# Optimization experiments

Hardware: AMD Instinct MI355X
Metric: run time of the kernel (lower is better)

## Reference

```python
import jax, jax.numpy as jnp
import numpy as np

EPS = 1e-5
B, NA, T, D, H, L, DFF, E = 4, 64, 128, 128, 8, 3, 512, 65536
NN = T * NA  # nodes per graph = t*n after reshape(b, t*n, f)
DH = D // H


def _layer_norm(x, g, b):
    m = x.mean(-1, keepdims=True)
    v = ((x - m) ** 2).mean(-1, keepdims=True)
    return (x - m) * jax.lax.rsqrt(v + EPS) * g + b


def _pos_encoding(t, d):
    pos = jnp.arange(t, dtype=jnp.float32)[:, None]
    i = jnp.arange(0, d, 2, dtype=jnp.float32)
    ang = pos * jnp.exp(-jnp.log(10000.0) * i / d)
    pe = jnp.zeros((t, d), jnp.float32)
    return pe.at[:, 0::2].set(jnp.sin(ang)).at[:, 1::2].set(jnp.cos(ang))


def _forward(all_hist_feat, edge_weight, hist_w, hist_b,
             attn_wq, attn_bq, attn_wk, attn_bk, attn_wv, attn_bv, attn_wo, attn_bo,
             ln1_g, ln1_b, ff_w1, ff_b1, ff_w2, ff_b2, ln2_g, ln2_b,
             bn_g, bn_b, lin_graph_w, lin_graph_b, edge_index):
    b, n, t, _ = all_hist_feat.shape
    # history embedding: Linear(3, D)  -> [b, n, t, D]
    x = all_hist_feat @ hist_w + hist_b
    # sinusoidal positional encoding over the time axis
    out_e = x + _pos_encoding(t, D)
    scale = 1.0 / jnp.sqrt(jnp.asarray(DH, jnp.float32))
    for l in range(L):  # small fixed layer count
        q = out_e @ attn_wq[l] + attn_bq[l]
        k = out_e @ attn_wk[l] + attn_bk[l]
        v = out_e @ attn_wv[l] + attn_bv[l]
        qh = q.reshape(b, n, t, H, DH)
        kh = k.reshape(b, n, t, H, DH)
        vh = v.reshape(b, n, t, H, DH)
        scores = jnp.einsum('bnqhd,bnkhd->bnhqk', qh, kh) * scale
        attn = jax.nn.softmax(scores, axis=-1)
        o = jnp.einsum('bnhqk,bnkhd->bnqhd', attn, vh).reshape(b, n, t, D)
        o = o @ attn_wo[l] + attn_bo[l]
        h1 = _layer_norm(out_e + o, ln1_g[l], ln1_b[l])
        ff = jax.nn.relu(h1 @ ff_w1[l] + ff_b1[l]) @ ff_w2[l] + ff_b2[l]
        out_e = _layer_norm(h1 + ff, ln2_g[l], ln2_b[l])
    # graph stage: nodes are (time, agent) pairs, index = time*n + agent
    graph_w = out_e.transpose(0, 2, 1, 3).reshape(b, t * n, D)
    graph_x = x.transpose(0, 2, 1, 3).reshape(b, t * n, D)
    # GCNConv_Fixed_W (no self loops, no normalize): per-node score then
    # edge-weighted scatter-add from source to target (PyG convention)
    s = (graph_w * graph_x).sum(-1)  # [b, t*n]
    src, dst = edge_index[:, 0], edge_index[:, 1]

    def agg(s_b, src_b, dst_b, ew_b):
        return jax.ops.segment_sum(ew_b * s_b[src_b], dst_b, num_segments=NN)

    graph_out = jax.vmap(agg)(s, src, dst, edge_weight)  # [b, t*n]
    g = graph_out.reshape(b, t, n)
    # BatchNorm2d(1) on [b, 1, n, t]: single channel -> global batch stats
    m = g.mean()
    var = g.var()
    g = (g - m) * jax.lax.rsqrt(var + EPS) * bn_g[0] + bn_b[0]
    g4 = g.transpose(0, 2, 1)[..., None]  # [b, n, t, 1]
    return g4 @ lin_graph_w + lin_graph_b  # [b, n, t, D]


def setup_inputs() -> dict:
    keys = iter(jax.random.split(jax.random.key(0), 64))

    def nrm(shape, scale):
        return jax.random.normal(next(keys), shape, jnp.float32) * scale

    inp = {
        'all_hist_feat': nrm((B, NA, T, 3), 1.0),
        'edge_index': jax.random.randint(next(keys), (B, 2, E), 0, NN, jnp.int32),
        'edge_weight': jax.random.uniform(next(keys), (B, E), jnp.float32),
        'hist_w': nrm((3, D), 0.5), 'hist_b': nrm((D,), 0.02),
        'attn_wq': nrm((L, D, D), D ** -0.5), 'attn_bq': jnp.zeros((L, D)),
        'attn_wk': nrm((L, D, D), D ** -0.5), 'attn_bk': jnp.zeros((L, D)),
        'attn_wv': nrm((L, D, D), D ** -0.5), 'attn_bv': jnp.zeros((L, D)),
        'attn_wo': nrm((L, D, D), D ** -0.5), 'attn_bo': jnp.zeros((L, D)),
        'ln1_g': jnp.ones((L, D)), 'ln1_b': jnp.zeros((L, D)),
        'ff_w1': nrm((L, D, DFF), D ** -0.5), 'ff_b1': jnp.zeros((L, DFF)),
        'ff_w2': nrm((L, DFF, D), DFF ** -0.5), 'ff_b2': jnp.zeros((L, D)),
        'ln2_g': jnp.ones((L, D)), 'ln2_b': jnp.zeros((L, D)),
        'bn_g': jnp.ones((1,)), 'bn_b': jnp.zeros((1,)),
        'lin_graph_w': nrm((1, D), 1.0), 'lin_graph_b': jnp.zeros((D,)),
    }
    return inp


def reference(all_hist_feat, edge_index, edge_weight, hist_w, hist_b,
              attn_wq, attn_bq, attn_wk, attn_bk, attn_wv, attn_bv, attn_wo, attn_bo,
              ln1_g, ln1_b, ff_w1, ff_b1, ff_w2, ff_b2, ln2_g, ln2_b,
              bn_g, bn_b, lin_graph_w, lin_graph_b):
    return _forward(all_hist_feat, edge_weight, hist_w, hist_b,
                    attn_wq, attn_bq, attn_wk, attn_bk, attn_wv, attn_bv, attn_wo, attn_bo,
                    ln1_g, ln1_b, ff_w1, ff_b1, ff_w2, ff_b2, ln2_g, ln2_b,
                    bn_g, bn_b, lin_graph_w, lin_graph_b, edge_index)
```

## Files before the change

kernel.cpp:

```cpp
#include <hip/hip_runtime.h>
#include <hip/hip_bf16.h>
#include <math.h>

#define EPS_ 1e-5f
constexpr int B_ = 4, NA = 64, T_ = 128, D_ = 128, H_ = 8, L_ = 3, DFF = 512, E_ = 65536;
constexpr int DH = D_ / H_;
constexpr int NN = T_ * NA;
constexpr int NTOT = B_ * NA * T_;
constexpr int QLD = 384;
constexpr size_t NE_ = (size_t)NTOT * D_;

typedef __bf16 bf16x8 __attribute__((ext_vector_type(8)));
typedef float f32x4 __attribute__((ext_vector_type(4)));

__global__ __launch_bounds__(256) void embed_kernel(
    const float* __restrict__ hist, const float* __restrict__ w,
    const float* __restrict__ b, float* __restrict__ x, float* __restrict__ e) {
  int idx = blockIdx.x * 256 + threadIdx.x;
  if (idx >= NTOT * D_) return;
  int d = idx & (D_ - 1);
  int r = idx >> 7;
  int t = r & (T_ - 1);
  const float* hp = hist + (size_t)r * 3;
  float acc = b[d];
  acc += hp[0] * w[0 * D_ + d];
  acc += hp[1] * w[1 * D_ + d];
  acc += hp[2] * w[2 * D_ + d];
  x[idx] = acc;
  int p = d >> 1;
  float ang = (float)t * expf(-logf(10000.f) * (2.f * (float)p) / (float)D_);
  float pe = (d & 1) ? cosf(ang) : sinf(ang);
  e[idx] = acc + pe;
}

__global__ __launch_bounds__(256) void convert_weights(
    const float* __restrict__ wq, const float* __restrict__ wk,
    const float* __restrict__ wv, const float* __restrict__ wo,
    const float* __restrict__ w1, const float* __restrict__ w2,
    __bf16* __restrict__ hi, __bf16* __restrict__ lo) {
  const int LW = 196608;
  int idx = blockIdx.x * 256 + threadIdx.x;
  if (idx >= L_ * LW) return;
  int l = idx / LW;
  int rem = idx - l * LW;
  float src;
  int n, k, K, segoff;
  if (rem < 49152) {
    n = rem >> 7; k = rem & 127; K = 128; segoff = 0;
    int which = n >> 7, nl = n & 127;
    const float* W = (which == 0) ? wq : (which == 1) ? wk : wv;
    src = W[(size_t)l * 16384 + k * 128 + nl];
  } else if (rem < 65536) {
    int r2 = rem - 49152;
    n = r2 >> 7; k = r2 & 127; K = 128; segoff = 49152;
    src = wo[(size_t)l * 16384 + k * 128 + n];
  } else if (rem < 131072) {
    int r2 = rem - 65536;
    n = r2 >> 7; k = r2 & 127; K = 128; segoff = 65536;
    src = w1[(size_t)l * 65536 + k * 512 + n];
  } else {
    int r2 = rem - 131072;
    n = r2 >> 9; k = r2 & 511; K = 512; segoff = 131072;
    src = w2[(size_t)l * 65536 + k * 128 + n];
  }
  int nt = n >> 4, kt = k >> 5;
  int lane = ((k >> 3) & 3) * 16 + (n & 15);
  int j = k & 7;
  int dst = l * LW + segoff + ((nt * (K / 32) + kt) * 64 + lane) * 8 + j;
  __bf16 h = (__bf16)src;
  hi[dst] = h;
  lo[dst] = (__bf16)(src - (float)h);
}

__global__ __launch_bounds__(256) void bias_pack(
    const float* __restrict__ bq, const float* __restrict__ bk,
    const float* __restrict__ bv, float* __restrict__ pb) {
  int idx = blockIdx.x * 256 + threadIdx.x;
  if (idx >= L_ * QLD) return;
  int l = idx / QLD, n = idx - l * QLD;
  int which = n >> 7, nl = n & 127;
  const float* src = (which == 0) ? bq : (which == 1) ? bk : bv;
  pb[idx] = src[l * 128 + nl];
}

__device__ __forceinline__ void split8(const float* __restrict__ p,
                                       bf16x8& hi, bf16x8& lo) {
  float4 x0 = *(const float4*)p;
  float4 x1 = *(const float4*)(p + 4);
  float xv[8] = {x0.x, x0.y, x0.z, x0.w, x1.x, x1.y, x1.z, x1.w};
#pragma unroll
  for (int j = 0; j < 8; ++j) {
    __bf16 h = (__bf16)xv[j];
    hi[j] = h;
    lo[j] = (__bf16)(xv[j] - (float)h);
  }
}

template <int EPI, int K>
__global__ __launch_bounds__(256) void gemm_big(
    const float* __restrict__ A, int lda,
    const __bf16* __restrict__ Whi, const __bf16* __restrict__ Wlo,
    const float* __restrict__ bias,
    float* __restrict__ C, int ldc) {
  const int wave = threadIdx.x >> 6;
  const int lane = threadIdx.x & 63;
  const int m16 = lane & 15;
  const int quad = lane >> 4;
  const int wrow = wave >> 1, wcol = wave & 1;
  const int row0 = blockIdx.y * 128 + wrow * 64;
  const int col0 = blockIdx.x * 128 + wcol * 64;
  const int ctb = col0 >> 4;

  f32x4 acc[4][4] = {};
#pragma unroll
  for (int k0 = 0; k0 < K; k0 += 32) {
    bf16x8 ahi[4], alo[4];
#pragma unroll
    for (int mf = 0; mf < 4; ++mf)
      split8(A + (size_t)(row0 + mf * 16 + m16) * lda + k0 + quad * 8, ahi[mf], alo[mf]);
    bf16x8 bhi[4], blo[4];
#pragma unroll
    for (int nf = 0; nf < 4; ++nf) {
      size_t off = ((size_t)(ctb + nf) * (K / 32) + (k0 >> 5)) * 512 + lane * 8;
      bhi[nf] = *(const bf16x8*)(Whi + off);
      blo[nf] = *(const bf16x8*)(Wlo + off);
    }
#pragma unroll
    for (int mf = 0; mf < 4; ++mf)
#pragma unroll
      for (int nf = 0; nf < 4; ++nf) {
        acc[mf][nf] = __builtin_amdgcn_mfma_f32_16x16x32_bf16(ahi[mf], bhi[nf], acc[mf][nf], 0, 0, 0);
        acc[mf][nf] = __builtin_amdgcn_mfma_f32_16x16x32_bf16(ahi[mf], blo[nf], acc[mf][nf], 0, 0, 0);
        acc[mf][nf] = __builtin_amdgcn_mfma_f32_16x16x32_bf16(alo[mf], bhi[nf], acc[mf][nf], 0, 0, 0);
      }
  }
#pragma unroll
  for (int mf = 0; mf < 4; ++mf)
#pragma unroll
    for (int nf = 0; nf < 4; ++nf) {
      int c = col0 + nf * 16 + m16;
      float bj = bias[c];
#pragma unroll
      for (int reg = 0; reg < 4; ++reg) {
        int r = row0 + mf * 16 + quad * 4 + reg;
        float v = acc[mf][nf][reg] + bj;
        if (EPI == 1) v = fmaxf(v, 0.f);
        C[(size_t)r * ldc + c] = v;
      }
    }
}

template <int K>
__global__ __launch_bounds__(256) void gemm_ln(
    const float* __restrict__ A, int lda,
    const __bf16* __restrict__ Whi, const __bf16* __restrict__ Wlo,
    const float* __restrict__ bias, const float* __restrict__ resid,
    const float* __restrict__ lng, const float* __restrict__ lnb,
    float* __restrict__ C) {
  const int wave = threadIdx.x >> 6;
  const int lane = threadIdx.x & 63;
  const int m16 = lane & 15;
  const int quad = lane >> 4;
  const int wrow = wave >> 1, wcol = wave & 1;
  const int row0 = blockIdx.y * 64 + wrow * 32;
  const int col0 = wcol * 64;
  const int ctb = wcol * 4;

  f32x4 acc[2][4] = {};
#pragma unroll
  for (int k0 = 0; k0 < K; k0 += 32) {
    bf16x8 ahi[2], alo[2];
#pragma unroll
    for (int mf = 0; mf < 2; ++mf)
      split8(A + (size_t)(row0 + mf * 16 + m16) * lda + k0 + quad * 8, ahi[mf], alo[mf]);
    bf16x8 bhi[4], blo[4];
#pragma unroll
    for (int nf = 0; nf < 4; ++nf) {
      size_t off = ((size_t)(ctb + nf) * (K / 32) + (k0 >> 5)) * 512 + lane * 8;
      bhi[nf] = *(const bf16x8*)(Whi + off);
      blo[nf] = *(const bf16x8*)(Wlo + off);
    }
#pragma unroll
    for (int mf = 0; mf < 2; ++mf)
#pragma unroll
      for (int nf = 0; nf < 4; ++nf) {
        acc[mf][nf] = __builtin_amdgcn_mfma_f32_16x16x32_bf16(ahi[mf], bhi[nf], acc[mf][nf], 0, 0, 0);
        acc[mf][nf] = __builtin_amdgcn_mfma_f32_16x16x32_bf16(ahi[mf], blo[nf], acc[mf][nf], 0, 0, 0);
        acc[mf][nf] = __builtin_amdgcn_mfma_f32_16x16x32_bf16(alo[mf], bhi[nf], acc[mf][nf], 0, 0, 0);
      }
  }
  __shared__ float rs[64][2], rq[64][2];
#pragma unroll
  for (int mf = 0; mf < 2; ++mf)
#pragma unroll
    for (int reg = 0; reg < 4; ++reg) {
      int lr = wrow * 32 + mf * 16 + quad * 4 + reg;
      int gr = blockIdx.y * 64 + lr;
      float s = 0.f, qq = 0.f;
#pragma unroll
      for (int nf = 0; nf < 4; ++nf) {
        int c = col0 + nf * 16 + m16;
        float v = acc[mf][nf][reg] + bias[c] + resid[(size_t)gr * 128 + c];
        acc[mf][nf][reg] = v;
        s += v;
        qq += v * v;
      }
#pragma unroll
      for (int off = 1; off < 16; off <<= 1) {
        s += __shfl_xor(s, off, 64);
        qq += __shfl_xor(qq, off, 64);
      }
      if (m16 == 0) { rs[lr][wcol] = s; rq[lr][wcol] = qq; }
    }
  __syncthreads();
#pragma unroll
  for (int mf = 0; mf < 2; ++mf)
#pragma unroll
    for (int reg = 0; reg < 4; ++reg) {
      int lr = wrow * 32 + mf * 16 + quad * 4 + reg;
      int gr = blockIdx.y * 64 + lr;
      float mean = (rs[lr][0] + rs[lr][1]) * (1.f / 128.f);
      float var = (rq[lr][0] + rq[lr][1]) * (1.f / 128.f) - mean * mean;
      float rstd = rsqrtf(var + EPS_);
#pragma unroll
      for (int nf = 0; nf < 4; ++nf) {
        int c = col0 + nf * 16 + m16;
        C[(size_t)gr * 128 + c] = (acc[mf][nf][reg] - mean) * rstd * lng[c] + lnb[c];
      }
    }
}

__global__ __launch_bounds__(256) void gemm_pk(
    const float* __restrict__ A, const __bf16* __restrict__ Whi,
    const __bf16* __restrict__ Wlo, float* __restrict__ P) {
  const int kc = blockIdx.x;
  const int wave = threadIdx.x >> 6;
  const int lane = threadIdx.x & 63;
  const int m16 = lane & 15;
  const int quad = lane >> 4;
  const int wrow = wave >> 1, wcol = wave & 1;
  const int row0 = blockIdx.y * 64 + wrow * 32;
  const int col0 = wcol * 64;
  const int ctb = wcol * 4;

  f32x4 acc[2][4] = {};
#pragma unroll
  for (int kt = 0; kt < 4; ++kt) {
    const int k0 = kc * 128 + kt * 32;
    bf16x8 ahi[2], alo[2];
#pragma unroll
    for (int mf = 0; mf < 2; ++mf)
      split8(A + (size_t)(row0 + mf * 16 + m16) * 512 + k0 + quad * 8, ahi[mf], alo[mf]);
    bf16x8 bhi[4], blo[4];
#pragma unroll
    for (int nf = 0; nf < 4; ++nf) {
      size_t off = ((size_t)(ctb + nf) * 16 + (k0 >> 5)) * 512 + lane * 8;
      bhi[nf] = *(const bf16x8*)(Whi + off);
      blo[nf] = *(const bf16x8*)(Wlo + off);
    }
#pragma unroll
    for (int mf = 0; mf < 2; ++mf)
#pragma unroll
      for (int nf = 0; nf < 4; ++nf) {
        acc[mf][nf] = __builtin_amdgcn_mfma_f32_16x16x32_bf16(ahi[mf], bhi[nf], acc[mf][nf], 0, 0, 0);
        acc[mf][nf] = __builtin_amdgcn_mfma_f32_16x16x32_bf16(ahi[mf], blo[nf], acc[mf][nf], 0, 0, 0);
        acc[mf][nf] = __builtin_amdgcn_mfma_f32_16x16x32_bf16(alo[mf], bhi[nf], acc[mf][nf], 0, 0, 0);
      }
  }
  float* out = P + (size_t)kc * NE_;
#pragma unroll
  for (int mf = 0; mf < 2; ++mf)
#pragma unroll
    for (int nf = 0; nf < 4; ++nf) {
      int c = col0 + nf * 16 + m16;
#pragma unroll
      for (int reg = 0; reg < 4; ++reg) {
        int r = row0 + mf * 16 + quad * 4 + reg;
        out[(size_t)r * 128 + c] = acc[mf][nf][reg];
      }
    }
}

__global__ __launch_bounds__(128) void reduce_ln4(
    const float* __restrict__ P, const float* __restrict__ bias,
    const float* __restrict__ resid,
    const float* __restrict__ gam, const float* __restrict__ bet,
    float* __restrict__ out) {
  int r = blockIdx.x;
  int d = threadIdx.x;
  size_t o = (size_t)r * D_ + d;
  float val = P[o] + P[o + NE_] + P[o + 2 * NE_] + P[o + 3 * NE_] + bias[d] + resid[o];
  __shared__ float red[4];
  float s = val;
#pragma unroll
  for (int off = 32; off; off >>= 1) s += __shfl_down(s, off, 64);
  if ((d & 63) == 0) red[d >> 6] = s;
  __syncthreads();
  float mean = (red[0] + red[1]) * (1.f / (float)D_);
  float dv = val - mean;
  float q = dv * dv;
#pragma unroll
  for (int off = 32; off; off >>= 1) q += __shfl_down(q, off, 64);
  if ((d & 63) == 0) red[2 + (d >> 6)] = q;
  __syncthreads();
  float var = (red[2] + red[3]) * (1.f / (float)D_);
  out[o] = dv * rsqrtf(var + EPS_) * gam[d] + bet[d];
}

__global__ __launch_bounds__(256) void attn_mfma(float* __restrict__ qkv) {
  const int h = blockIdx.x & (H_ - 1);
  const int bn = blockIdx.x >> 3;
  const int wave = threadIdx.x >> 6;
  const int lane = threadIdx.x & 63;
  const int m16 = lane & 15;
  const int quad = lane >> 4;
  const int row0 = wave * 32;
  const float* Qb = qkv + (size_t)bn * T_ * QLD + h * DH;
  const float* Kb = Qb + 128;
  const float* Vb = Qb + 256;
  float* Ob = (float*)Vb;

  __shared__ __bf16 Plds[4][32][136];

  bf16x8 qhi[2], qlo[2];
#pragma unroll
  for (int mf = 0; mf < 2; ++mf) {
    if (quad < 2) {
      split8(Qb + (size_t)(row0 + mf * 16 + m16) * QLD + quad * 8, qhi[mf], qlo[mf]);
    } else {
#pragma unroll
      for (int j = 0; j < 8; ++j) { qhi[mf][j] = (__bf16)0.f; qlo[mf][j] = (__bf16)0.f; }
    }
  }

  f32x4 acc[2][8] = {};
#pragma unroll
  for (int nf = 0; nf < 8; ++nf) {
    bf16x8 khi, klo;
    if (quad < 2) {
      split8(Kb + (size_t)(nf * 16 + m16) * QLD + quad * 8, khi, klo);
    } else {
#pragma unroll
      for (int j = 0; j < 8; ++j) { khi[j] = (__bf16)0.f; klo[j] = (__bf16)0.f; }
    }
#pragma unroll
    for (int mf = 0; mf < 2; ++mf) {
      acc[mf][nf] = __builtin_amdgcn_mfma_f32_16x16x32_bf16(qhi[mf], khi, acc[mf][nf], 0, 0, 0);
      acc[mf][nf] = __builtin_amdgcn_mfma_f32_16x16x32_bf16(qhi[mf], klo, acc[mf][nf], 0, 0, 0);
      acc[mf][nf] = __builtin_amdgcn_mfma_f32_16x16x32_bf16(qlo[mf], khi, acc[mf][nf], 0, 0, 0);
    }
  }

  const float scale = 0.25f;
#pragma unroll
  for (int mf = 0; mf < 2; ++mf)
#pragma unroll
    for (int reg = 0; reg < 4; ++reg) {
      float mx = -1e30f;
#pragma unroll
      for (int nf = 0; nf < 8; ++nf) mx = fmaxf(mx, acc[mf][nf][reg]);
#pragma unroll
      for (int off = 1; off < 16; off <<= 1) mx = fmaxf(mx, __shfl_xor(mx, off, 64));
      float sum = 0.f;
#pragma unroll
      for (int nf = 0; nf < 8; ++nf) {
        float e = __expf((acc[mf][nf][reg] - mx) * scale);
        acc[mf][nf][reg] = e;
        sum += e;
      }
#pragma unroll
      for (int off = 1; off < 16; off <<= 1) sum += __shfl_xor(sum, off, 64);
      float inv = 1.f / sum;
#pragma unroll
      for (int nf = 0; nf < 8; ++nf) acc[mf][nf][reg] *= inv;
    }

#pragma unroll
  for (int mf = 0; mf < 2; ++mf)
#pragma unroll
    for (int nf = 0; nf < 8; ++nf)
#pragma unroll
      for (int reg = 0; reg < 4; ++reg)
        Plds[wave][mf * 16 + quad * 4 + reg][nf * 16 + m16] = (__bf16)acc[mf][nf][reg];

  f32x4 oacc[2] = {};
#pragma unroll
  for (int kc = 0; kc < 4; ++kc) {
    bf16x8 pa0 = *(const bf16x8*)&Plds[wave][m16][kc * 32 + quad * 8];
    bf16x8 pa1 = *(const bf16x8*)&Plds[wave][16 + m16][kc * 32 + quad * 8];
    bf16x8 vhi, vlo;
#pragma unroll
    for (int j = 0; j < 8; ++j) {
      float x = Vb[(size_t)(kc * 32 + quad * 8 + j) * QLD + m16];
      __bf16 hh = (__bf16)x;
      vhi[j] = hh;
      vlo[j] = (__bf16)(x - (float)hh);
    }
    oacc[0] = __builtin_amdgcn_mfma_f32_16x16x32_bf16(pa0, vhi, oacc[0], 0, 0, 0);
    oacc[0] = __builtin_amdgcn_mfma_f32_16x16x32_bf16(pa0, vlo, oacc[0], 0, 0, 0);
    oacc[1] = __builtin_amdgcn_mfma_f32_16x16x32_bf16(pa1, vhi, oacc[1], 0, 0, 0);
    oacc[1] = __builtin_amdgcn_mfma_f32_16x16x32_bf16(pa1, vlo, oacc[1], 0, 0, 0);
  }

  __syncthreads();
#pragma unroll
  for (int mf = 0; mf < 2; ++mf)
#pragma unroll
    for (int reg = 0; reg < 4; ++reg) {
      int r = row0 + mf * 16 + quad * 4 + reg;
      Ob[(size_t)r * QLD + m16] = oacc[mf][reg];
    }
}

__global__ __launch_bounds__(256) void sdot_kernel(
    const float* __restrict__ e, const float* __restrict__ x, float* __restrict__ s) {
  int r = blockIdx.x * 4 + (threadIdx.x >> 6);
  int lane = threadIdx.x & 63;
  const float* ep = e + (size_t)r * D_;
  const float* xp = x + (size_t)r * D_;
  float acc = ep[lane] * xp[lane] + ep[lane + 64] * xp[lane + 64];
#pragma unroll
  for (int off = 32; off; off >>= 1) acc += __shfl_down(acc, off, 64);
  if (lane == 0) {
    int t = r & (T_ - 1);
    int bn = r >> 7;
    int n = bn & (NA - 1);
    int b = bn >> 6;
    s[(size_t)b * NN + t * NA + n] = acc;
  }
}

__global__ __launch_bounds__(256) void scatter_kernel(
    const float* __restrict__ s, const int* __restrict__ ei,
    const float* __restrict__ ew, float* __restrict__ g) {
  int idx = blockIdx.x * 256 + threadIdx.x;
  if (idx >= B_ * E_) return;
  int b = idx >> 16;
  int e = idx & (E_ - 1);
  int src = ei[(size_t)b * 2 * E_ + e];
  int dst = ei[(size_t)b * 2 * E_ + E_ + e];
  float w = ew[(size_t)b * E_ + e];
  atomicAdd(&g[(size_t)b * NN + dst], w * s[(size_t)b * NN + src]);
}

__global__ __launch_bounds__(256) void stats_partial(
    const float* __restrict__ g, float* __restrict__ st) {
  int i = blockIdx.x * 256 + threadIdx.x;
  float v = g[i];
  float sum = v, sq = v * v;
#pragma unroll
  for (int off = 32; off; off >>= 1) {
    sum += __shfl_down(sum, off, 64);
    sq += __shfl_down(sq, off, 64);
  }
  __shared__ float s1[4], s2[4];
  int w = threadIdx.x >> 6;
  if ((threadIdx.x & 63) == 0) { s1[w] = sum; s2[w] = sq; }
  __syncthreads();
  if (threadIdx.x == 0) {
    atomicAdd(&st[0], s1[0] + s1[1] + s1[2] + s1[3]);
    atomicAdd(&st[1], s2[0] + s2[1] + s2[2] + s2[3]);
  }
}

__global__ __launch_bounds__(256) void final_kernel(
    const float* __restrict__ g, const float* __restrict__ st,
    const float* __restrict__ bng, const float* __restrict__ bnb,
    const float* __restrict__ lw, const float* __restrict__ lb,
    float* __restrict__ out) {
  int idx = blockIdx.x * 256 + threadIdx.x;
  if (idx >= NTOT * D_) return;
  int d = idx & (D_ - 1);
  int r = idx >> 7;
  int t = r & (T_ - 1);
  int bn = r >> 7;
  int n = bn & (NA - 1);
  int b = bn >> 6;
  const float invn = 1.f / (float)(B_ * NN);
  float m = st[0] * invn;
  float var = st[1] * invn - m * m;
  float rs = rsqrtf(var + EPS_);
  float gv = g[(size_t)b * NN + t * NA + n];
  float val = (gv - m) * rs * bng[0] + bnb[0];
  out[idx] = val * lw[d] + lb[d];
}

extern "C" void kernel_launch(void* const* d_in, const int* in_sizes, int n_in,
                              void* d_out, int out_size, void* d_ws, size_t ws_size,
                              hipStream_t stream) {
  const float* hist = (const float*)d_in[0];
  const int* eidx = (const int*)d_in[1];
  const float* ew = (const float*)d_in[2];
  const float* hw = (const float*)d_in[3];
  const float* hb = (const float*)d_in[4];
  const float* wq = (const float*)d_in[5];
  const float* bq = (const float*)d_in[6];
  const float* wk = (const float*)d_in[7];
  const float* bk = (const float*)d_in[8];
  const float* wv = (const float*)d_in[9];
  const float* bv = (const float*)d_in[10];
  const float* wo = (const float*)d_in[11];
  const float* bo = (const float*)d_in[12];
  const float* ln1g = (const float*)d_in[13];
  const float* ln1b = (const float*)d_in[14];
  const float* w1 = (const float*)d_in[15];
  const float* b1 = (const float*)d_in[16];
  const float* w2 = (const float*)d_in[17];
  const float* b2 = (const float*)d_in[18];
  const float* ln2g = (const float*)d_in[19];
  const float* ln2b = (const float*)d_in[20];
  const float* bng = (const float*)d_in[21];
  const float* bnb = (const float*)d_in[22];
  const float* lgw = (const float*)d_in[23];
  const float* lgb = (const float*)d_in[24];
  float* out = (float*)d_out;

  float* ws = (float*)d_ws;
  const size_t NE = NE_;
  float* bx = ws + 0 * NE;
  float* be = ws + 1 * NE;
  float* h1 = ws + 2 * NE;
  float* qkv = ws + 3 * NE;
  float* ffmid = ws + 3 * NE;
  float* pk_ = ws + 7 * NE;
  float* bs_ = ws + 11 * NE;
  float* bg_ = bs_ + NTOT;
  float* bst = bg_ + NTOT;
  float* pbias = bst + 2;
  const int LW = 196608;
  __bf16* whiB = (__bf16*)(pbias + L_ * QLD);
  __bf16* wloB = whiB + (size_t)L_ * LW;

  convert_weights<<<(L_ * LW + 255) / 256, 256, 0, stream>>>(
      wq, wk, wv, wo, w1, w2, whiB, wloB);
  bias_pack<<<(L_ * QLD + 255) / 256, 256, 0, stream>>>(bq, bk, bv, pbias);
  embed_kernel<<<(NTOT * D_) / 256, 256, 0, stream>>>(hist, hw, hb, bx, be);

  for (int l = 0; l < L_; ++l) {
    const __bf16* hiL = whiB + (size_t)l * LW;
    const __bf16* loL = wloB + (size_t)l * LW;
    gemm_big<0, 128><<<dim3(3, NTOT / 128), 256, 0, stream>>>(
        be, 128, hiL, loL, pbias + l * QLD, qkv, QLD);
    attn_mfma<<<B_ * NA * H_, 256, 0, stream>>>(qkv);
    gemm_ln<128><<<dim3(1, NTOT / 64), 256, 0, stream>>>(
        qkv + 256, QLD, hiL + 49152, loL + 49152, bo + l * D_, be,
        ln1g + l * D_, ln1b + l * D_, h1);
    gemm_big<1, 128><<<dim3(4, NTOT / 128), 256, 0, stream>>>(
        h1, 128, hiL + 65536, loL + 65536, b1 + l * DFF, ffmid, 512);
    gemm_pk<<<dim3(4, NTOT / 64), 256, 0, stream>>>(
        ffmid, hiL + 131072, loL + 131072, pk_);
    reduce_ln4<<<NTOT, 128, 0, stream>>>(
        pk_, b2 + l * D_, h1, ln2g + l * D_, ln2b + l * D_, be);
  }

  sdot_kernel<<<NTOT / 4, 256, 0, stream>>>(be, bx, bs_);
  hipMemsetAsync(bg_, 0, ((size_t)B_ * NN + 2) * sizeof(float), stream);
  scatter_kernel<<<(B_ * E_) / 256, 256, 0, stream>>>(bs_, eidx, ew, bg_);
  stats_partial<<<(B_ * NN) / 256, 256, 0, stream>>>(bg_, bst);
  final_kernel<<<(NTOT * D_) / 256, 256, 0, stream>>>(bg_, bst, bng, bnb, lgw, lgb, out);
}
```

Baseline: 606.2 us.

## Fuse FF2 split-K GEMM with bias, residual and LayerNorm into one kernel

New measurement: 555.4 us. 8.4% less time.

```diff
diff --git a/kernel.cpp b/kernel.cpp
--- a/kernel.cpp
+++ b/kernel.cpp
@@ -230,81 +230,100 @@
     }
 }
 
-__global__ __launch_bounds__(256) void gemm_pk(
-    const float* __restrict__ A, const __bf16* __restrict__ Whi,
-    const __bf16* __restrict__ Wlo, float* __restrict__ P) {
-  const int kc = blockIdx.x;
+__global__ __launch_bounds__(256) void ff2_ln(
+    const float* __restrict__ A,
+    const __bf16* __restrict__ Whi, const __bf16* __restrict__ Wlo,
+    const float* __restrict__ bias, const float* __restrict__ resid,
+    const float* __restrict__ lng, const float* __restrict__ lnb,
+    float* __restrict__ C) {
   const int wave = threadIdx.x >> 6;
   const int lane = threadIdx.x & 63;
   const int m16 = lane & 15;
   const int quad = lane >> 4;
   const int wrow = wave >> 1, wcol = wave & 1;
-  const int row0 = blockIdx.y * 64 + wrow * 32;
+  const int grow0 = blockIdx.y * 64;
+  const int lrow0 = wrow * 32;
   const int col0 = wcol * 64;
   const int ctb = wcol * 4;
 
+  __shared__ float As[64][129];
+
   f32x4 acc[2][4] = {};
-#pragma unroll
-  for (int kt = 0; kt < 4; ++kt) {
-    const int k0 = kc * 128 + kt * 32;
-    bf16x8 ahi[2], alo[2];
-#pragma unroll
-    for (int mf = 0; mf < 2; ++mf)
-      split8(A + (size_t)(row0 + mf * 16 + m16) * 512 + k0 + quad * 8, ahi[mf], alo[mf]);
-    bf16x8 bhi[4], blo[4];
-#pragma unroll
-    for (int nf = 0; nf < 4; ++nf) {
-      size_t off = ((size_t)(ctb + nf) * 16 + (k0 >> 5)) * 512 + lane * 8;
-      bhi[nf] = *(const bf16x8*)(Whi + off);
-      blo[nf] = *(const bf16x8*)(Wlo + off);
-    }
-#pragma unroll
-    for (int mf = 0; mf < 2; ++mf)
-#pragma unroll
-      for (int nf = 0; nf < 4; ++nf) {
-        acc[mf][nf] = __builtin_amdgcn_mfma_f32_16x16x32_bf16(ahi[mf], bhi[nf], acc[mf][nf], 0, 0, 0);
-        acc[mf][nf] = __builtin_amdgcn_mfma_f32_16x16x32_bf16(ahi[mf], blo[nf], acc[mf][nf], 0, 0, 0);
-        acc[mf][nf] = __builtin_amdgcn_mfma_f32_16x16x32_bf16(alo[mf], bhi[nf], acc[mf][nf], 0, 0, 0);
-      }
-  }
-  float* out = P + (size_t)kc * NE_;
-#pragma unroll
-  for (int mf = 0; mf < 2; ++mf)
-#pragma unroll
-    for (int nf = 0; nf < 4; ++nf) {
-      int c = col0 + nf * 16 + m16;
-#pragma unroll
-      for (int reg = 0; reg < 4; ++reg) {
-        int r = row0 + mf * 16 + quad * 4 + reg;
-        out[(size_t)r * 128 + c] = acc[mf][nf][reg];
-      }
-    }
-}
-
-__global__ __launch_bounds__(128) void reduce_ln4(
-    const float* __restrict__ P, const float* __restrict__ bias,
-    const float* __restrict__ resid,
-    const float* __restrict__ gam, const float* __restrict__ bet,
-    float* __restrict__ out) {
-  int r = blockIdx.x;
-  int d = threadIdx.x;
-  size_t o = (size_t)r * D_ + d;
-  float val = P[o] + P[o + NE_] + P[o + 2 * NE_] + P[o + 3 * NE_] + bias[d] + resid[o];
-  __shared__ float red[4];
-  float s = val;
-#pragma unroll
-  for (int off = 32; off; off >>= 1) s += __shfl_down(s, off, 64);
-  if ((d & 63) == 0) red[d >> 6] = s;
+  for (int kc = 0; kc < 4; ++kc) {
+    if (kc) __syncthreads();
+#pragma unroll
+    for (int u = 0; u < 8; ++u) {
+      int unit = threadIdx.x + u * 256;
+      int r = unit >> 5, c4 = unit & 31;
+      float4 v = *(const float4*)(A + (size_t)(grow0 + r) * 512 + kc * 128 + c4 * 4);
+      As[r][c4 * 4 + 0] = v.x;
+      As[r][c4 * 4 + 1] = v.y;
+      As[r][c4 * 4 + 2] = v.z;
+      As[r][c4 * 4 + 3] = v.w;
+    }
+    __syncthreads();
+#pragma unroll
+    for (int kt = 0; kt < 4; ++kt) {
+      bf16x8 ahi[2], alo[2];
+#pragma unroll
+      for (int mf = 0; mf < 2; ++mf)
+        split8(&As[lrow0 + mf * 16 + m16][kt * 32 + quad * 8], ahi[mf], alo[mf]);
+      bf16x8 bhi[4], blo[4];
+#pragma unroll
+      for (int nf = 0; nf < 4; ++nf) {
+        size_t off = ((size_t)(ctb + nf) * 16 + (kc * 4 + kt)) * 512 + lane * 8;
+        bhi[nf] = *(const bf16x8*)(Whi + off);
+        blo[nf] = *(const bf16x8*)(Wlo + off);
+      }
+#pragma unroll
+      for (int mf = 0; mf < 2; ++mf)
+#pragma unroll
+        for (int nf = 0; nf < 4; ++nf) {
+          acc[mf][nf] = __builtin_amdgcn_mfma_f32_16x16x32_bf16(ahi[mf], bhi[nf], acc[mf][nf], 0, 0, 0);
+          acc[mf][nf] = __builtin_amdgcn_mfma_f32_16x16x32_bf16(ahi[mf], blo[nf], acc[mf][nf], 0, 0, 0);
+          acc[mf][nf] = __builtin_amdgcn_mfma_f32_16x16x32_bf16(alo[mf], bhi[nf], acc[mf][nf], 0, 0, 0);
+        }
+    }
+  }
+  __shared__ float rs[64][2], rq[64][2];
+#pragma unroll
+  for (int mf = 0; mf < 2; ++mf)
+#pragma unroll
+    for (int reg = 0; reg < 4; ++reg) {
+      int lr = lrow0 + mf * 16 + quad * 4 + reg;
+      int gr = grow0 + lr;
+      float s = 0.f, qq = 0.f;
+#pragma unroll
+      for (int nf = 0; nf < 4; ++nf) {
+        int c = col0 + nf * 16 + m16;
+        float v = acc[mf][nf][reg] + bias[c] + resid[(size_t)gr * 128 + c];
+        acc[mf][nf][reg] = v;
+        s += v;
+        qq += v * v;
+      }
+#pragma unroll
+      for (int off = 1; off < 16; off <<= 1) {
+        s += __shfl_xor(s, off, 64);
+        qq += __shfl_xor(qq, off, 64);
+      }
+      if (m16 == 0) { rs[lr][wcol] = s; rq[lr][wcol] = qq; }
+    }
   __syncthreads();
-  float mean = (red[0] + red[1]) * (1.f / (float)D_);
-  float dv = val - mean;
-  float q = dv * dv;
-#pragma unroll
-  for (int off = 32; off; off >>= 1) q += __shfl_down(q, off, 64);
-  if ((d & 63) == 0) red[2 + (d >> 6)] = q;
-  __syncthreads();
-  float var = (red[2] + red[3]) * (1.f / (float)D_);
-  out[o] = dv * rsqrtf(var + EPS_) * gam[d] + bet[d];
+#pragma unroll
+  for (int mf = 0; mf < 2; ++mf)
+#pragma unroll
+    for (int reg = 0; reg < 4; ++reg) {
+      int lr = lrow0 + mf * 16 + quad * 4 + reg;
+      int gr = grow0 + lr;
+      float mean = (rs[lr][0] + rs[lr][1]) * (1.f / 128.f);
+      float var = (rq[lr][0] + rq[lr][1]) * (1.f / 128.f) - mean * mean;
+      float rstd = rsqrtf(var + EPS_);
+#pragma unroll
+      for (int nf = 0; nf < 4; ++nf) {
+        int c = col0 + nf * 16 + m16;
+        C[(size_t)gr * 128 + c] = (acc[mf][nf][reg] - mean) * rstd * lng[c] + lnb[c];
+      }
+    }
 }
 
 __global__ __launch_bounds__(256) void attn_mfma(float* __restrict__ qkv) {
@@ -522,8 +541,7 @@
   float* h1 = ws + 2 * NE;
   float* qkv = ws + 3 * NE;
   float* ffmid = ws + 3 * NE;
-  float* pk_ = ws + 7 * NE;
-  float* bs_ = ws + 11 * NE;
+  float* bs_ = ws + 7 * NE;
   float* bg_ = bs_ + NTOT;
   float* bst = bg_ + NTOT;
   float* pbias = bst + 2;
@@ -547,10 +565,9 @@
         ln1g + l * D_, ln1b + l * D_, h1);
     gemm_big<1, 128><<<dim3(4, NTOT / 128), 256, 0, stream>>>(
         h1, 128, hiL + 65536, loL + 65536, b1 + l * DFF, ffmid, 512);
-    gemm_pk<<<dim3(4, NTOT / 64), 256, 0, stream>>>(
-        ffmid, hiL + 131072, loL + 131072, pk_);
-    reduce_ln4<<<NTOT, 128, 0, stream>>>(
-        pk_, b2 + l * D_, h1, ln2g + l * D_, ln2b + l * D_, be);
+    ff2_ln<<<dim3(1, NTOT / 64), 256, 0, stream>>>(
+        ffmid, hiL + 131072, loL + 131072, b2 + l * D_, h1,
+        ln2g + l * D_, ln2b + l * D_, be);
   }
 
   sdot_kernel<<<NTOT / 4, 256, 0, stream>>>(be, bx, bs_);
```
